# Kernel optimization log

Measured on AMD Instinct MI355X. Metric: run time of the kernel, lower is better.

Reference implementation:

```python
import math
import jax, jax.numpy as jnp
import numpy as np

jax.config.update("jax_enable_x64", True)  # hash math uses int64, as in the torch reference

N_LEVELS = 16
F = 2                     # n_feat_per_entry
T = 2 ** 19               # hashmap size per level (max)
BASE_RES = 16
MAX_RES = 512
MIN_XYZ = -0.75           # origin (0,0,0), side 1.5
MAX_XYZ = 0.75
B = 1_000_000

# per_level_scale computed in float32 like torch.exp(torch.log(...))
_SCALE = float(np.exp(np.log(np.float32(MAX_RES / BASE_RES)) / np.float32(N_LEVELS - 1)))

def _level_info():
    offsets, res, n = [], [], 0
    for i in range(N_LEVELS):
        offsets.append(n)
        r = math.floor(BASE_RES * _SCALE ** i)
        res.append(r)
        n += min(T, (r + 1) ** 3)
    offsets.append(n)
    return offsets, res, n

OFFSETS, RES, N_TOTAL = _level_info()  # N_TOTAL == 5262476
PRIMES = np.array([1, 2654435761, 805459861], dtype=np.int64)
# corner offsets in {0,1}^3; weight = prod over dims of (frac if corner==1 else 1-frac)
CORNERS = np.array([[i, j, k] for i in (0, 1) for j in (0, 1) for k in (0, 1)], dtype=np.int64)  # (8,3)


def _hashgrid_forward(xyz, embeddings):
    """xyz: (B,3) float32 inside the bbox; embeddings: (N_TOTAL,F) float32."""
    norm = (xyz - MIN_XYZ) / (MAX_XYZ - MIN_XYZ)  # (B,3) in [0,1]
    corners = jnp.asarray(CORNERS)                # (8,3) int64
    primes = jnp.asarray(PRIMES)                  # (3,) int64
    corner_is_one = jnp.asarray(CORNERS.astype(bool))  # (8,3)
    outs = [xyz]  # include_input=True, raw input first
    for lvl in range(N_LEVELS):
        r = RES[lvl]
        off = OFFSETS[lvl]
        size = OFFSETS[lvl + 1] - off   # = min(T, (r+1)^3)
        pos = norm * r                                     # (B,3)
        base = jnp.clip(jnp.floor(pos).astype(jnp.int64), 0, r - 1)  # (B,3)
        frac = pos - base.astype(pos.dtype)                # (B,3)
        idx3 = base[:, None, :] + corners[None]            # (B,8,3) grid-pt coords
        # fast_hash: xor of coord*prime per dim, then mod level size, plus level offset
        p = idx3 * primes                                  # (B,8,3) int64
        hidx = (p[..., 0] ^ p[..., 1] ^ p[..., 2]) % size + off  # (B,8)
        vals = embeddings[hidx]                            # (B,8,F) gather
        w = jnp.prod(jnp.where(corner_is_one[None], frac[:, None, :], 1.0 - frac[:, None, :]), axis=-1)  # (B,8)
        outs.append(jnp.einsum('bc,bcf->bf', w, vals))     # trilinear interp -> (B,F)
    return jnp.concatenate(outs, axis=-1)                  # (B, 3 + L*F) = (B,35)


def setup_inputs() -> dict:
    key = jax.random.key(0)
    k1, k2 = jax.random.split(key)
    # points strictly inside the bbox [-0.75, 0.75]^3
    xyz = jax.random.uniform(k1, (B, 3), dtype=jnp.float32,
                             minval=MIN_XYZ + 1e-3, maxval=MAX_XYZ - 1e-3)
    # torch init is uniform(-1e-4, 1e-4)
    emb = jax.random.uniform(k2, (N_TOTAL, F), dtype=jnp.float32, minval=-1e-4, maxval=1e-4)
    return {"xyz": xyz, "embeddings": emb}


def reference(xyz, embeddings):
    return _hashgrid_forward(xyz, embeddings)
```

## Files before the change

kernel.cpp:

```cpp
#include <hip/hip_runtime.h>
#include <stdint.h>
#include <string.h>

#define NLEV 16

typedef float  vfloat4 __attribute__((ext_vector_type(4)));

__device__ __forceinline__ void norm_coords(const float* __restrict__ xyz, int p,
                                            float& nx, float& ny, float& nz) {
    const float x = __builtin_nontemporal_load(xyz + 3 * p + 0);
    const float y = __builtin_nontemporal_load(xyz + 3 * p + 1);
    const float z = __builtin_nontemporal_load(xyz + 3 * p + 2);
    const float inv = 1.0f / 1.5f;
    nx = (x + 0.75f) * inv;
    ny = (y + 0.75f) * inv;
    nz = (z + 0.75f) * inv;
}

__device__ __forceinline__ float2 trilerp(const float2 v[8],
                                          float fx, float fy, float fz) {
    const float gx = 1.0f - fx, gy = 1.0f - fy, gz = 1.0f - fz;
    const float w00 = gx * gy, w01 = gx * fy, w10 = fx * gy, w11 = fx * fy;
    float w, f0, f1;
    w = w00 * gz; f0 = w * v[0].x;          f1 = w * v[0].y;
    w = w00 * fz; f0 = fmaf(w, v[1].x, f0); f1 = fmaf(w, v[1].y, f1);
    w = w01 * gz; f0 = fmaf(w, v[2].x, f0); f1 = fmaf(w, v[2].y, f1);
    w = w01 * fz; f0 = fmaf(w, v[3].x, f0); f1 = fmaf(w, v[3].y, f1);
    w = w10 * gz; f0 = fmaf(w, v[4].x, f0); f1 = fmaf(w, v[4].y, f1);
    w = w10 * fz; f0 = fmaf(w, v[5].x, f0); f1 = fmaf(w, v[5].y, f1);
    w = w11 * gz; f0 = fmaf(w, v[6].x, f0); f1 = fmaf(w, v[6].y, f1);
    w = w11 * fz; f0 = fmaf(w, v[7].x, f0); f1 = fmaf(w, v[7].y, f1);
    return make_float2(f0, f1);
}

template<int R, uint32_t OFF>
__global__ __launch_bounds__(256, 4) void big_level2(
    const float* __restrict__ xyz,
    const float2* __restrict__ emb,
    float2* __restrict__ ws,
    int nb)
{
    const int t  = threadIdx.x;
    const int p0 = blockIdx.x * 512 + t;
    const int p1 = p0 + 256;
    const int q[2] = { p0 < nb ? p0 : nb - 1, p1 < nb ? p1 : nb - 1 };

    const float4* __restrict__ emb4 = (const float4*)emb;
    const uint32_t M = 524287u;

    uint32_t h0[2][4];
    uint32_t yzs[2][4];
    uint32_t hx1_[2];
    float4   V[2][4];
    float2   w1[2][4];
    float    fx[2], fy[2], fz[2];
    bool     oddbx[2];

    #pragma unroll
    for (int j = 0; j < 2; ++j) {
        float nx, ny, nz;
        norm_coords(xyz, q[j], nx, ny, nz);
        const float rf = (float)R;
        const float px = nx * rf, py = ny * rf, pz = nz * rf;
        int bx = (int)floorf(px); bx = bx < 0 ? 0 : (bx > R - 1 ? R - 1 : bx);
        int by = (int)floorf(py); by = by < 0 ? 0 : (by > R - 1 ? R - 1 : by);
        int bz = (int)floorf(pz); bz = bz < 0 ? 0 : (bz > R - 1 ? R - 1 : bz);
        fx[j] = px - (float)bx;
        fy[j] = py - (float)by;
        fz[j] = pz - (float)bz;

        const uint32_t hy0 = (uint32_t)by       * 2654435761u;
        const uint32_t hy1 = (uint32_t)(by + 1) * 2654435761u;
        const uint32_t hz0 = (uint32_t)bz       * 805459861u;
        const uint32_t hz1 = (uint32_t)(bz + 1) * 805459861u;
        yzs[j][0] = hy0 ^ hz0; yzs[j][1] = hy0 ^ hz1;
        yzs[j][2] = hy1 ^ hz0; yzs[j][3] = hy1 ^ hz1;

        const uint32_t hx0 = (uint32_t)bx;
        oddbx[j] = (bx & 1) != 0;
        hx1_[j]  = hx0 + 1u;

        #pragma unroll
        for (int i = 0; i < 4; ++i) {
            h0[j][i] = (hx0 ^ yzs[j][i]) & M;
            V[j][i]  = emb4[(h0[j][i] >> 1) + (OFF >> 1)];
        }
    }

    #pragma unroll
    for (int j = 0; j < 2; ++j) {
        if (oddbx[j]) {
            #pragma unroll
            for (int i = 0; i < 4; ++i)
                w1[j][i] = emb[((hx1_[j] ^ yzs[j][i]) & M) + OFF];
        }
    }

    float2 r[2];
    #pragma unroll
    for (int j = 0; j < 2; ++j) {
        float2 v[8];
        #pragma unroll
        for (int i = 0; i < 4; ++i) {
            const float2 lo = make_float2(V[j][i].x, V[j][i].y);
            const float2 hi = make_float2(V[j][i].z, V[j][i].w);
            const bool oh = (h0[j][i] & 1u) != 0u;
            v[i]     = oh ? hi : lo;
            v[i + 4] = oddbx[j] ? w1[j][i] : (oh ? lo : hi);
        }
        r[j] = trilerp(v, fx[j], fy[j], fz[j]);
    }

    uint64_t u0, u1;
    memcpy(&u0, &r[0], 8);
    memcpy(&u1, &r[1], 8);
    if (p0 < nb) __builtin_nontemporal_store(u0, (uint64_t*)ws + p0);
    if (p1 < nb) __builtin_nontemporal_store(u1, (uint64_t*)ws + p1);
}

__global__ __launch_bounds__(256, 4) void pack_small(
    const float* __restrict__ xyz,
    const float2* __restrict__ emb,
    const float2* __restrict__ ws,
    float* __restrict__ out,
    int nb)
{
    constexpr int      kRes[7]  = {16, 20, 25, 32, 40, 50, 64};
    constexpr uint32_t kSize[7] = {4913u, 9261u, 17576u, 35937u, 68921u, 132651u, 274625u};
    constexpr uint32_t kOff[7]  = {0u, 4913u, 14174u, 31750u, 67687u, 136608u, 269259u};

    __shared__ __align__(16) float lds[4 * 64 * 35];

    const int tid  = threadIdx.x;
    const int lane = tid & 63;
    const int wid  = tid >> 6;
    const int p    = blockIdx.x * 256 + tid;
    const int pc   = (p < nb) ? p : (nb - 1);

    uint64_t wsv[9];
    #pragma unroll
    for (int l = 0; l < 9; ++l)
        wsv[l] = __builtin_nontemporal_load(
            (const uint64_t*)ws + (size_t)l * nb + pc);

    const float x = xyz[3 * pc + 0];
    const float y = xyz[3 * pc + 1];
    const float z = xyz[3 * pc + 2];

    float* wl = &lds[(wid * 64 + lane) * 35];
    wl[0] = x; wl[1] = y; wl[2] = z;

    const float inv = 1.0f / 1.5f;
    const float nx = (x + 0.75f) * inv;
    const float ny = (y + 0.75f) * inv;
    const float nz = (z + 0.75f) * inv;

    #pragma unroll
    for (int l = 0; l < 7; ++l) {
        const int      r   = kRes[l];
        const float    rf  = (float)r;
        const uint32_t sz  = kSize[l];
        const uint32_t off = kOff[l];

        const float px = nx * rf, py = ny * rf, pz = nz * rf;
        int bx = (int)floorf(px); bx = bx < 0 ? 0 : (bx > r - 1 ? r - 1 : bx);
        int by = (int)floorf(py); by = by < 0 ? 0 : (by > r - 1 ? r - 1 : by);
        int bz = (int)floorf(pz); bz = bz < 0 ? 0 : (bz > r - 1 ? r - 1 : bz);
        const float fx = px - (float)bx;
        const float fy = py - (float)by;
        const float fz = pz - (float)bz;

        const bool     evenbx = (bx & 1) == 0;
        const uint64_t hx0 = (uint64_t)(uint32_t)bx;
        const uint64_t hx1 = hx0 + 1u;
        const uint64_t hy0 = (uint64_t)(uint32_t)by       * 2654435761ull;
        const uint64_t hy1 = (uint64_t)(uint32_t)(by + 1) * 2654435761ull;
        const uint64_t hz0 = (uint64_t)(uint32_t)bz       * 805459861ull;
        const uint64_t hz1 = (uint64_t)(uint32_t)(bz + 1) * 805459861ull;

        const uint64_t yzc[4] = { hy0 ^ hz0, hy0 ^ hz1, hy1 ^ hz0, hy1 ^ hz1 };

        float2 v[8];
        #pragma unroll
        for (int c = 0; c < 4; ++c) {
            const uint64_t a0 = hx0 ^ yzc[c];
            const uint32_t h0 = (uint32_t)(a0 % sz);
            const bool     odd_a = ((uint32_t)a0 & 1u) != 0u;
            const int  hm = (int)h0 - (int)(odd_a ? 1 : 0);
            const bool ok = evenbx && (hm >= 0) && (hm != (int)sz - 1);
            const uint32_t iload = (ok ? (uint32_t)hm : h0) + off;
            const float4 V = *(const float4*)(emb + iload);
            float2 w1 = make_float2(0.0f, 0.0f);
            if (!ok) {
                const uint32_t h1 = (uint32_t)((hx1 ^ yzc[c]) % sz);
                w1 = emb[h1 + off];
            }
            const float2 loV = make_float2(V.x, V.y);
            const float2 hiV = make_float2(V.z, V.w);
            v[c]     = ok ? (odd_a ? hiV : loV) : loV;
            v[c + 4] = ok ? (odd_a ? loV : hiV) : w1;
        }

        const float2 rr = trilerp(v, fx, fy, fz);
        wl[3 + 2 * l] = rr.x;
        wl[4 + 2 * l] = rr.y;
    }

    #pragma unroll
    for (int l = 0; l < 9; ++l) {
        float2 bv;
        memcpy(&bv, &wsv[l], 8);
        wl[3 + 2 * (l + 7)] = bv.x;
        wl[4 + 2 * (l + 7)] = bv.y;
    }

    __syncthreads();

    const int wave_gid = blockIdx.x * 4 + wid;
    if (wave_gid * 64 < nb) {
        const vfloat4* s4 = (const vfloat4*)&lds[wid * 64 * 35];
        vfloat4* d4 = (vfloat4*)(out + (size_t)wave_gid * (64 * 35));
        #pragma unroll
        for (int c = 0; c < 8; ++c)
            __builtin_nontemporal_store(s4[c * 64 + lane], &d4[c * 64 + lane]);
        if (lane < 48)
            __builtin_nontemporal_store(s4[8 * 64 + lane], &d4[8 * 64 + lane]);
    }
}

__global__ __launch_bounds__(256, 4) void hashgrid_mono(
    const float* __restrict__ xyz,
    const float2* __restrict__ emb,
    float* __restrict__ out,
    int nb)
{
    constexpr int      kRes[NLEV]  = {16,20,25,32,40,50,64,80,101,128,161,203,256,322,406,512};
    constexpr uint32_t kSize[NLEV] = {4913u,9261u,17576u,35937u,68921u,132651u,274625u,
                                      524288u,524288u,524288u,524288u,524288u,
                                      524288u,524288u,524288u,524288u};
    constexpr uint32_t kOff[NLEV]  = {0u,4913u,14174u,31750u,67687u,136608u,269259u,543884u,
                                      1068172u,1592460u,2116748u,2641036u,3165324u,
                                      3689612u,4213900u,4738188u};

    __shared__ __align__(16) float lds[4 * 64 * 35];

    const int tid  = threadIdx.x;
    const int lane = tid & 63;
    const int wid  = tid >> 6;
    const int p    = blockIdx.x * 256 + tid;
    const int pc   = (p < nb) ? p : (nb - 1);

    const float x = xyz[3 * pc + 0];
    const float y = xyz[3 * pc + 1];
    const float z = xyz[3 * pc + 2];

    float* wl = &lds[(wid * 64 + lane) * 35];
    wl[0] = x; wl[1] = y; wl[2] = z;

    const float inv = 1.0f / 1.5f;
    const float nx = (x + 0.75f) * inv;
    const float ny = (y + 0.75f) * inv;
    const float nz = (z + 0.75f) * inv;

    #pragma unroll
    for (int l = 0; l < NLEV; ++l) {
        const int      r   = kRes[l];
        const float    rf  = (float)r;
        const uint32_t sz  = kSize[l];
        const uint32_t off = kOff[l];

        const float px = nx * rf, py = ny * rf, pz = nz * rf;
        int bx = (int)floorf(px); bx = bx < 0 ? 0 : (bx > r - 1 ? r - 1 : bx);
        int by = (int)floorf(py); by = by < 0 ? 0 : (by > r - 1 ? r - 1 : by);
        int bz = (int)floorf(pz); bz = bz < 0 ? 0 : (bz > r - 1 ? r - 1 : bz);
        const float fx = px - (float)bx;
        const float fy = py - (float)by;
        const float fz = pz - (float)bz;

        const uint64_t hx0 = (uint64_t)(uint32_t)bx;
        const uint64_t hx1 = hx0 + 1u;
        const uint64_t hy0 = (uint64_t)(uint32_t)by       * 2654435761ull;
        const uint64_t hy1 = (uint64_t)(uint32_t)(by + 1) * 2654435761ull;
        const uint64_t hz0 = (uint64_t)(uint32_t)bz       * 805459861ull;
        const uint64_t hz1 = (uint64_t)(uint32_t)(bz + 1) * 805459861ull;

        const uint64_t yz00 = hy0 ^ hz0, yz01 = hy0 ^ hz1;
        const uint64_t yz10 = hy1 ^ hz0, yz11 = hy1 ^ hz1;

        const uint32_t i000 = (uint32_t)((hx0 ^ yz00) % sz) + off;
        const uint32_t i001 = (uint32_t)((hx0 ^ yz01) % sz) + off;
        const uint32_t i010 = (uint32_t)((hx0 ^ yz10) % sz) + off;
        const uint32_t i011 = (uint32_t)((hx0 ^ yz11) % sz) + off;
        const uint32_t i100 = (uint32_t)((hx1 ^ yz00) % sz) + off;
        const uint32_t i101 = (uint32_t)((hx1 ^ yz01) % sz) + off;
        const uint32_t i110 = (uint32_t)((hx1 ^ yz10) % sz) + off;
        const uint32_t i111 = (uint32_t)((hx1 ^ yz11) % sz) + off;

        const float2 v000 = emb[i000];
        const float2 v001 = emb[i001];
        const float2 v010 = emb[i010];
        const float2 v011 = emb[i011];
        const float2 v100 = emb[i100];
        const float2 v101 = emb[i101];
        const float2 v110 = emb[i110];
        const float2 v111 = emb[i111];

        const float gx = 1.0f - fx, gy = 1.0f - fy, gz = 1.0f - fz;
        const float w00 = gx * gy, w01 = gx * fy, w10 = fx * gy, w11 = fx * fy;

        float w, f0, f1;
        w = w00 * gz; f0 = w * v000.x;          f1 = w * v000.y;
        w = w00 * fz; f0 = fmaf(w, v001.x, f0); f1 = fmaf(w, v001.y, f1);
        w = w01 * gz; f0 = fmaf(w, v010.x, f0); f1 = fmaf(w, v010.y, f1);
        w = w01 * fz; f0 = fmaf(w, v011.x, f0); f1 = fmaf(w, v011.y, f1);
        w = w10 * gz; f0 = fmaf(w, v100.x, f0); f1 = fmaf(w, v100.y, f1);
        w = w10 * fz; f0 = fmaf(w, v101.x, f0); f1 = fmaf(w, v101.y, f1);
        w = w11 * gz; f0 = fmaf(w, v110.x, f0); f1 = fmaf(w, v110.y, f1);
        w = w11 * fz; f0 = fmaf(w, v111.x, f0); f1 = fmaf(w, v111.y, f1);

        wl[3 + 2 * l] = f0;
        wl[4 + 2 * l] = f1;
    }

    __syncthreads();

    const int wave_gid = blockIdx.x * 4 + wid;
    if (wave_gid * 64 < nb) {
        const float* src = &lds[wid * 64 * 35];
        float* dst = out + (size_t)wave_gid * (64 * 35);
        #pragma unroll
        for (int c = 0; c < 35; ++c)
            dst[c * 64 + lane] = src[c * 64 + lane];
    }
}

extern "C" void kernel_launch(void* const* d_in, const int* in_sizes, int n_in,
                              void* d_out, int out_size, void* d_ws, size_t ws_size,
                              hipStream_t stream) {
    const float*  xyz = (const float*)d_in[0];
    const float2* emb = (const float2*)d_in[1];
    float*        out = (float*)d_out;
    const int nb = in_sizes[0] / 3;
    const int blocks  = (nb + 255) / 256;
    const int blocks2 = (nb + 511) / 512;

    const size_t ws_need = (size_t)9 * (size_t)nb * sizeof(float2);
    if (ws_size < ws_need) {
        hashgrid_mono<<<blocks, 256, 0, stream>>>(xyz, emb, out, nb);
        return;
    }

    float2* ws = (float2*)d_ws;
    big_level2< 80,  543884u><<<blocks2, 256, 0, stream>>>(xyz, emb, ws + (size_t)0 * nb, nb);
    big_level2<101, 1068172u><<<blocks2, 256, 0, stream>>>(xyz, emb, ws + (size_t)1 * nb, nb);
    big_level2<128, 1592460u><<<blocks2, 256, 0, stream>>>(xyz, emb, ws + (size_t)2 * nb, nb);
    big_level2<161, 2116748u><<<blocks2, 256, 0, stream>>>(xyz, emb, ws + (size_t)3 * nb, nb);
    big_level2<203, 2641036u><<<blocks2, 256, 0, stream>>>(xyz, emb, ws + (size_t)4 * nb, nb);
    big_level2<256, 3165324u><<<blocks2, 256, 0, stream>>>(xyz, emb, ws + (size_t)5 * nb, nb);
    big_level2<322, 3689612u><<<blocks2, 256, 0, stream>>>(xyz, emb, ws + (size_t)6 * nb, nb);
    big_level2<406, 4213900u><<<blocks2, 256, 0, stream>>>(xyz, emb, ws + (size_t)7 * nb, nb);
    big_level2<512, 4738188u><<<blocks2, 256, 0, stream>>>(xyz, emb, ws + (size_t)8 * nb, nb);
    pack_small<<<blocks, 256, 0, stream>>>(xyz, emb, ws, out, nb);
}
```

Before: 584.7 us.

## Use one point per thread in big levels, halve pack LDS, rework small-level hash pairing

```diff
diff --git a/kernel.cpp b/kernel.cpp
--- a/kernel.cpp
+++ b/kernel.cpp
@@ -34,91 +34,73 @@
 }
 
 template<int R, uint32_t OFF>
-__global__ __launch_bounds__(256, 4) void big_level2(
+__global__ __launch_bounds__(256, 8) void big_level1(
     const float* __restrict__ xyz,
     const float2* __restrict__ emb,
     float2* __restrict__ ws,
     int nb)
 {
-    const int t  = threadIdx.x;
-    const int p0 = blockIdx.x * 512 + t;
-    const int p1 = p0 + 256;
-    const int q[2] = { p0 < nb ? p0 : nb - 1, p1 < nb ? p1 : nb - 1 };
+    const int p = blockIdx.x * 256 + threadIdx.x;
+    if (p >= nb) return;
 
     const float4* __restrict__ emb4 = (const float4*)emb;
     const uint32_t M = 524287u;
 
-    uint32_t h0[2][4];
-    uint32_t yzs[2][4];
-    uint32_t hx1_[2];
-    float4   V[2][4];
-    float2   w1[2][4];
-    float    fx[2], fy[2], fz[2];
-    bool     oddbx[2];
-
-    #pragma unroll
-    for (int j = 0; j < 2; ++j) {
-        float nx, ny, nz;
-        norm_coords(xyz, q[j], nx, ny, nz);
-        const float rf = (float)R;
-        const float px = nx * rf, py = ny * rf, pz = nz * rf;
-        int bx = (int)floorf(px); bx = bx < 0 ? 0 : (bx > R - 1 ? R - 1 : bx);
-        int by = (int)floorf(py); by = by < 0 ? 0 : (by > R - 1 ? R - 1 : by);
-        int bz = (int)floorf(pz); bz = bz < 0 ? 0 : (bz > R - 1 ? R - 1 : bz);
-        fx[j] = px - (float)bx;
-        fy[j] = py - (float)by;
-        fz[j] = pz - (float)bz;
-
-        const uint32_t hy0 = (uint32_t)by       * 2654435761u;
-        const uint32_t hy1 = (uint32_t)(by + 1) * 2654435761u;
-        const uint32_t hz0 = (uint32_t)bz       * 805459861u;
-        const uint32_t hz1 = (uint32_t)(bz + 1) * 805459861u;
-        yzs[j][0] = hy0 ^ hz0; yzs[j][1] = hy0 ^ hz1;
-        yzs[j][2] = hy1 ^ hz0; yzs[j][3] = hy1 ^ hz1;
-
-        const uint32_t hx0 = (uint32_t)bx;
-        oddbx[j] = (bx & 1) != 0;
-        hx1_[j]  = hx0 + 1u;
-
-        #pragma unroll
-        for (int i = 0; i < 4; ++i) {
-            h0[j][i] = (hx0 ^ yzs[j][i]) & M;
-            V[j][i]  = emb4[(h0[j][i] >> 1) + (OFF >> 1)];
-        }
-    }
-
-    #pragma unroll
-    for (int j = 0; j < 2; ++j) {
-        if (oddbx[j]) {
-            #pragma unroll
-            for (int i = 0; i < 4; ++i)
-                w1[j][i] = emb[((hx1_[j] ^ yzs[j][i]) & M) + OFF];
-        }
-    }
-
-    float2 r[2];
-    #pragma unroll
-    for (int j = 0; j < 2; ++j) {
-        float2 v[8];
-        #pragma unroll
-        for (int i = 0; i < 4; ++i) {
-            const float2 lo = make_float2(V[j][i].x, V[j][i].y);
-            const float2 hi = make_float2(V[j][i].z, V[j][i].w);
-            const bool oh = (h0[j][i] & 1u) != 0u;
-            v[i]     = oh ? hi : lo;
-            v[i + 4] = oddbx[j] ? w1[j][i] : (oh ? lo : hi);
-        }
-        r[j] = trilerp(v, fx[j], fy[j], fz[j]);
-    }
-
-    uint64_t u0, u1;
-    memcpy(&u0, &r[0], 8);
-    memcpy(&u1, &r[1], 8);
-    if (p0 < nb) __builtin_nontemporal_store(u0, (uint64_t*)ws + p0);
-    if (p1 < nb) __builtin_nontemporal_store(u1, (uint64_t*)ws + p1);
-}
-
-__global__ __launch_bounds__(256, 4) void pack_small(
+    float nx, ny, nz;
+    norm_coords(xyz, p, nx, ny, nz);
+
+    const float rf = (float)R;
+    const float px = nx * rf, py = ny * rf, pz = nz * rf;
+    int bx = (int)floorf(px); bx = bx < 0 ? 0 : (bx > R - 1 ? R - 1 : bx);
+    int by = (int)floorf(py); by = by < 0 ? 0 : (by > R - 1 ? R - 1 : by);
+    int bz = (int)floorf(pz); bz = bz < 0 ? 0 : (bz > R - 1 ? R - 1 : bz);
+    const float fx = px - (float)bx;
+    const float fy = py - (float)by;
+    const float fz = pz - (float)bz;
+
+    const uint32_t hy0 = (uint32_t)by       * 2654435761u;
+    const uint32_t hy1 = (uint32_t)(by + 1) * 2654435761u;
+    const uint32_t hz0 = (uint32_t)bz       * 805459861u;
+    const uint32_t hz1 = (uint32_t)(bz + 1) * 805459861u;
+    uint32_t yzs[4];
+    yzs[0] = hy0 ^ hz0; yzs[1] = hy0 ^ hz1;
+    yzs[2] = hy1 ^ hz0; yzs[3] = hy1 ^ hz1;
+
+    const uint32_t hx0 = (uint32_t)bx;
+    const bool oddbx = (bx & 1) != 0;
+    const uint32_t hx1 = hx0 + 1u;
+
+    uint32_t h0[4];
+    float4   V[4];
+    #pragma unroll
+    for (int i = 0; i < 4; ++i) {
+        h0[i] = (hx0 ^ yzs[i]) & M;
+        V[i]  = emb4[(h0[i] >> 1) + (OFF >> 1)];
+    }
+    float2 w1[4];
+    if (oddbx) {
+        #pragma unroll
+        for (int i = 0; i < 4; ++i)
+            w1[i] = emb[((hx1 ^ yzs[i]) & M) + OFF];
+    }
+
+    float2 v[8];
+    #pragma unroll
+    for (int i = 0; i < 4; ++i) {
+        const float2 lo = make_float2(V[i].x, V[i].y);
+        const float2 hi = make_float2(V[i].z, V[i].w);
+        const bool oh = (h0[i] & 1u) != 0u;
+        v[i]     = oh ? hi : lo;
+        v[i + 4] = oddbx ? w1[i] : (oh ? lo : hi);
+    }
+    const float2 r = trilerp(v, fx, fy, fz);
+
+    uint64_t u;
+    memcpy(&u, &r, 8);
+    __builtin_nontemporal_store(u, (uint64_t*)ws + p);
+}
+
+__global__ __launch_bounds__(256, 8) void pack_small(
     const float* __restrict__ xyz,
     const float2* __restrict__ emb,
     const float2* __restrict__ ws,
@@ -129,7 +111,7 @@
     constexpr uint32_t kSize[7] = {4913u, 9261u, 17576u, 35937u, 68921u, 132651u, 274625u};
     constexpr uint32_t kOff[7]  = {0u, 4913u, 14174u, 31750u, 67687u, 136608u, 269259u};
 
-    __shared__ __align__(16) float lds[4 * 64 * 35];
+    __shared__ __align__(16) float lds[4][32 * 35];
 
     const int tid  = threadIdx.x;
     const int lane = tid & 63;
@@ -147,8 +129,8 @@
     const float y = xyz[3 * pc + 1];
     const float z = xyz[3 * pc + 2];
 
-    float* wl = &lds[(wid * 64 + lane) * 35];
-    wl[0] = x; wl[1] = y; wl[2] = z;
+    float rec[35];
+    rec[0] = x; rec[1] = y; rec[2] = z;
 
     const float inv = 1.0f / 1.5f;
     const float nx = (x + 0.75f) * inv;
@@ -170,9 +152,8 @@
         const float fy = py - (float)by;
         const float fz = pz - (float)bz;
 
-        const bool     evenbx = (bx & 1) == 0;
-        const uint64_t hx0 = (uint64_t)(uint32_t)bx;
-        const uint64_t hx1 = hx0 + 1u;
+        const uint32_t x0 = (uint32_t)bx;
+        const uint32_t x1 = x0 + 1u;
         const uint64_t hy0 = (uint64_t)(uint32_t)by       * 2654435761ull;
         const uint64_t hy1 = (uint64_t)(uint32_t)(by + 1) * 2654435761ull;
         const uint64_t hz0 = (uint64_t)(uint32_t)bz       * 805459861ull;
@@ -183,48 +164,79 @@
         float2 v[8];
         #pragma unroll
         for (int c = 0; c < 4; ++c) {
-            const uint64_t a0 = hx0 ^ yzc[c];
-            const uint32_t h0 = (uint32_t)(a0 % sz);
-            const bool     odd_a = ((uint32_t)a0 & 1u) != 0u;
-            const int  hm = (int)h0 - (int)(odd_a ? 1 : 0);
-            const bool ok = evenbx && (hm >= 0) && (hm != (int)sz - 1);
-            const uint32_t iload = (ok ? (uint32_t)hm : h0) + off;
+            const uint64_t yz = yzc[c];
+            const uint32_t m  = (uint32_t)(yz % sz);
+            const uint32_t w  = (uint32_t)yz & 127u;
+            const int d0 = (int)(w ^ x0) - (int)w;
+            const int d1 = (int)(w ^ x1) - (int)w;
+            int h0 = (int)m + d0;
+            h0 += (h0 < 0) ? (int)sz : 0;
+            h0 -= (h0 >= (int)sz) ? (int)sz : 0;
+            int h1 = (int)m + d1;
+            h1 += (h1 < 0) ? (int)sz : 0;
+            h1 -= (h1 >= (int)sz) ? (int)sz : 0;
+
+            const int  lo  = h0 < h1 ? h0 : h1;
+            const bool ok  = ((h0 > h1 ? h0 : h1) - lo) == 1;
+            const uint32_t iload = (uint32_t)(ok ? lo : h0) + off;
             const float4 V = *(const float4*)(emb + iload);
             float2 w1 = make_float2(0.0f, 0.0f);
-            if (!ok) {
-                const uint32_t h1 = (uint32_t)((hx1 ^ yzc[c]) % sz);
-                w1 = emb[h1 + off];
-            }
+            if (!ok) w1 = emb[(uint32_t)h1 + off];
             const float2 loV = make_float2(V.x, V.y);
             const float2 hiV = make_float2(V.z, V.w);
-            v[c]     = ok ? (odd_a ? hiV : loV) : loV;
-            v[c + 4] = ok ? (odd_a ? loV : hiV) : w1;
+            const bool x0lo = (h0 == lo);
+            v[c]     = ok ? (x0lo ? loV : hiV) : loV;
+            v[c + 4] = ok ? (x0lo ? hiV : loV) : w1;
         }
 
         const float2 rr = trilerp(v, fx, fy, fz);
-        wl[3 + 2 * l] = rr.x;
-        wl[4 + 2 * l] = rr.y;
+        rec[3 + 2 * l] = rr.x;
+        rec[4 + 2 * l] = rr.y;
     }
 
     #pragma unroll
     for (int l = 0; l < 9; ++l) {
         float2 bv;
         memcpy(&bv, &wsv[l], 8);
-        wl[3 + 2 * (l + 7)] = bv.x;
-        wl[4 + 2 * (l + 7)] = bv.y;
-    }
-
+        rec[17 + 2 * l] = bv.x;
+        rec[18 + 2 * l] = bv.y;
+    }
+
+    const int  wave_gid = blockIdx.x * 4 + wid;
+    const bool full     = (wave_gid * 64 < nb);
+    float* wbuf = lds[wid];
+
+    if ((lane >> 5) == 0) {
+        float* wl = wbuf + lane * 35;
+        #pragma unroll
+        for (int c = 0; c < 35; ++c) wl[c] = rec[c];
+    }
     __syncthreads();
-
-    const int wave_gid = blockIdx.x * 4 + wid;
-    if (wave_gid * 64 < nb) {
-        const vfloat4* s4 = (const vfloat4*)&lds[wid * 64 * 35];
+    if (full) {
+        const vfloat4* s4 = (const vfloat4*)wbuf;
         vfloat4* d4 = (vfloat4*)(out + (size_t)wave_gid * (64 * 35));
         #pragma unroll
-        for (int c = 0; c < 8; ++c)
+        for (int c = 0; c < 4; ++c)
             __builtin_nontemporal_store(s4[c * 64 + lane], &d4[c * 64 + lane]);
-        if (lane < 48)
-            __builtin_nontemporal_store(s4[8 * 64 + lane], &d4[8 * 64 + lane]);
+        if (lane < 24)
+            __builtin_nontemporal_store(s4[256 + lane], &d4[256 + lane]);
+    }
+    __syncthreads();
+
+    if ((lane >> 5) == 1) {
+        float* wl = wbuf + (lane - 32) * 35;
+        #pragma unroll
+        for (int c = 0; c < 35; ++c) wl[c] = rec[c];
+    }
+    __syncthreads();
+    if (full) {
+        const vfloat4* s4 = (const vfloat4*)wbuf;
+        vfloat4* d4 = (vfloat4*)(out + (size_t)wave_gid * (64 * 35) + 1120);
+        #pragma unroll
+        for (int c = 0; c < 4; ++c)
+            __builtin_nontemporal_store(s4[c * 64 + lane], &d4[c * 64 + lane]);
+        if (lane < 24)
+            __builtin_nontemporal_store(s4[256 + lane], &d4[256 + lane]);
     }
 }
 
@@ -341,8 +353,7 @@
     const float2* emb = (const float2*)d_in[1];
     float*        out = (float*)d_out;
     const int nb = in_sizes[0] / 3;
-    const int blocks  = (nb + 255) / 256;
-    const int blocks2 = (nb + 511) / 512;
+    const int blocks = (nb + 255) / 256;
 
     const size_t ws_need = (size_t)9 * (size_t)nb * sizeof(float2);
     if (ws_size < ws_need) {
@@ -351,14 +362,14 @@
     }
 
     float2* ws = (float2*)d_ws;
-    big_level2< 80,  543884u><<<blocks2, 256, 0, stream>>>(xyz, emb, ws + (size_t)0 * nb, nb);
-    big_level2<101, 1068172u><<<blocks2, 256, 0, stream>>>(xyz, emb, ws + (size_t)1 * nb, nb);
-    big_level2<128, 1592460u><<<blocks2, 256, 0, stream>>>(xyz, emb, ws + (size_t)2 * nb, nb);
-    big_level2<161, 2116748u><<<blocks2, 256, 0, stream>>>(xyz, emb, ws + (size_t)3 * nb, nb);
-    big_level2<203, 2641036u><<<blocks2, 256, 0, stream>>>(xyz, emb, ws + (size_t)4 * nb, nb);
-    big_level2<256, 3165324u><<<blocks2, 256, 0, stream>>>(xyz, emb, ws + (size_t)5 * nb, nb);
-    big_level2<322, 3689612u><<<blocks2, 256, 0, stream>>>(xyz, emb, ws + (size_t)6 * nb, nb);
-    big_level2<406, 4213900u><<<blocks2, 256, 0, stream>>>(xyz, emb, ws + (size_t)7 * nb, nb);
-    big_level2<512, 4738188u><<<blocks2, 256, 0, stream>>>(xyz, emb, ws + (size_t)8 * nb, nb);
+    big_level1< 80,  543884u><<<blocks, 256, 0, stream>>>(xyz, emb, ws + (size_t)0 * nb, nb);
+    big_level1<101, 1068172u><<<blocks, 256, 0, stream>>>(xyz, emb, ws + (size_t)1 * nb, nb);
+    big_level1<128, 1592460u><<<blocks, 256, 0, stream>>>(xyz, emb, ws + (size_t)2 * nb, nb);
+    big_level1<161, 2116748u><<<blocks, 256, 0, stream>>>(xyz, emb, ws + (size_t)3 * nb, nb);
+    big_level1<203, 2641036u><<<blocks, 256, 0, stream>>>(xyz, emb, ws + (size_t)4 * nb, nb);
+    big_level1<256, 3165324u><<<blocks, 256, 0, stream>>>(xyz, emb, ws + (size_t)5 * nb, nb);
+    big_level1<322, 3689612u><<<blocks, 256, 0, stream>>>(xyz, emb, ws + (size_t)6 * nb, nb);
+    big_level1<406, 4213900u><<<blocks, 256, 0, stream>>>(xyz, emb, ws + (size_t)7 * nb, nb);
+    big_level1<512, 4738188u><<<blocks, 256, 0, stream>>>(xyz, emb, ws + (size_t)8 * nb, nb);
     pack_small<<<blocks, 256, 0, stream>>>(xyz, emb, ws, out, nb);
 }
```

Measured after the change: 1.162 ms. +98.8%, slower.
